# Performance work log

Measured on AMD Instinct MI355X. Metric: run time of the kernel, lower is better.

Reference implementation:

```python
import jax, jax.numpy as jnp
import numpy as np

N = 30000   # fluid particles
E = 480000  # edges
F = 4       # fluidFeatures (in channels)
P = 8       # RBF basis size per dim (dims=[8], 1D)
LAYERS = [32, 64, 64, 2]


def hat_basis(x, n):
    # 'linear' RBF: hat functions on n evenly spaced centers in [-1, 1]
    centers = jnp.linspace(-1.0, 1.0, n, dtype=x.dtype)
    spacing = 2.0 / (n - 1)
    return jnp.maximum(0.0, 1.0 - jnp.abs(x[:, None] - centers[None, :]) / spacing)  # [E, n]


def rbf_conv(x, fi, fj, d, W, b, mask, n_nodes):
    # x: [N, Cin]; d: [E, 1] clamped; W: [P, Cin, Cout]; b: [Cout]
    phi = hat_basis(d[:, 0], W.shape[0])      # [E, P]
    xj = x[fj]                                 # gather source features [E, Cin]
    msg = jnp.zeros((xj.shape[0], W.shape[2]), dtype=x.dtype)
    for p in range(W.shape[0]):                # small fixed P=8 loop keeps memory O(E*Cout)
        msg = msg + phi[:, p, None] * (xj @ W[p])
    msg = jnp.where(mask[:, None], msg, 0.0)   # centerIgnore: drop self edges fi==fj
    out = jax.ops.segment_sum(msg, fi, num_segments=n_nodes)  # scatter-reduce to targets
    return out + b


def _xavier(key, shape_in, shape_out):
    lim = float(np.sqrt(6.0 / (shape_in + shape_out)))
    return jax.random.uniform(key, (shape_in, shape_out), jnp.float32, -lim, lim)


def setup_inputs() -> dict:
    key = jax.random.key(0)
    ks = jax.random.split(key, 16)
    fluidFeatures = jax.random.normal(ks[0], (N, F), jnp.float32)
    fi = jax.random.randint(ks[1], (E,), 0, N)
    fj = jax.random.randint(ks[2], (E,), 0, N)
    distances = jax.random.normal(ks[3], (E, 1), jnp.float32)
    # conv channels: 4->32, 64->64, 64->64, 64->2
    cio = [(F, 32), (2 * 32, 64), (64, 64), (64, 2)]
    inp = {"fluidFeatures": fluidFeatures, "fi": fi, "fj": fj, "distances": distances}
    for li, (ci, co) in enumerate(cio):
        inp[f"cW{li}"] = jax.random.normal(ks[4 + li], (P, ci, co), jnp.float32) * (1.0 / np.sqrt(P * ci))
        inp[f"cb{li}"] = jnp.zeros((co,), jnp.float32)
        inp[f"fW{li}"] = _xavier(ks[8 + li], ci, co)   # stored [in, out]
        inp[f"fb{li}"] = jnp.zeros((co,), jnp.float32)
    return inp


def reference(fluidFeatures, fi, fj, distances,
              cW0, cb0, fW0, fb0, cW1, cb1, fW1, fb1,
              cW2, cb2, fW2, fb2, cW3, cb3, fW3, fb3):
    n_nodes = fluidFeatures.shape[0]
    mask = fi != fj                     # centerIgnore (mask instead of filter: jit-safe)
    d = jnp.clip(distances, -1.0, 1.0)

    conv0 = rbf_conv(fluidFeatures, fi, fj, d, cW0, cb0, mask, n_nodes)  # [N, 32]
    lin0 = fluidFeatures @ fW0 + fb0                                      # [N, 32]
    ans = jnp.concatenate([lin0, conv0], axis=1)                          # [N, 64]

    # i = 1: features[0]=32 != features[1]=64 -> no residual
    ansc = jax.nn.relu(ans)
    ans = rbf_conv(ansc, fi, fj, d, cW1, cb1, mask, n_nodes) + (ansc @ fW1 + fb1)
    # i = 2: features[1]==features[2]==64 and shapes match -> residual
    ansc = jax.nn.relu(ans)
    ans = rbf_conv(ansc, fi, fj, d, cW2, cb2, mask, n_nodes) + (ansc @ fW2 + fb2) + ans
    # i = 3: 64 -> 2, no residual
    ansc = jax.nn.relu(ans)
    ans = rbf_conv(ansc, fi, fj, d, cW3, cb3, mask, n_nodes) + (ansc @ fW3 + fb3)

    return ans  # dim == 1 (dims=[8]) -> no /128
```

## Files before the change

### kernel.cpp

```cpp
#include <hip/hip_runtime.h>


#define CAP 48

typedef __attribute__((ext_vector_type(8))) short short8;
typedef __attribute__((ext_vector_type(4))) short short4v;
typedef __attribute__((ext_vector_type(4))) float f32x4;

__device__ __forceinline__ short bf16s(float f) {
  unsigned u = __float_as_uint(f);
  return (short)((u + 0x7FFF + ((u >> 16) & 1)) >> 16);
}
__device__ __forceinline__ float b2f(unsigned short s) {
  return __uint_as_float(((unsigned)s) << 16);
}

__global__ void fill_kernel(const float* __restrict__ dist,
                            const int* __restrict__ fi, const int* __restrict__ fj,
                            int* __restrict__ cnt, int* __restrict__ jw, int nE) {
  int e = blockIdx.x * blockDim.x + threadIdx.x;
  if (e >= nE) return;
  int i = fi[e], j = fj[e];
  if (i == j) return;
  float d = fminf(1.0f, fmaxf(-1.0f, dist[e]));
  float u = (d + 1.0f) * 3.5f;
  int p = min((int)u, 6);
  float w0 = 1.0f - (u - (float)p);
  int wq = (int)(w0 * 16383.0f + 0.5f);
  int pos = atomicAdd(&cnt[i], 1);
  if (pos < CAP)
    jw[(size_t)i * CAP + pos] = j | (p << 15) | (wq << 18);
}

__global__ void prep_wtul(const float* __restrict__ cW1, const float* __restrict__ fW1,
                          const float* __restrict__ cW2, const float* __restrict__ fW2,
                          short* __restrict__ wt1, short* __restrict__ wt2) {
  int idx = blockIdx.x * blockDim.x + threadIdx.x;
  if (idx >= 2 * 576 * 64) return;
  int sel = idx / (576 * 64);
  int r = idx - sel * (576 * 64);
  int col = r >> 6, ch = r & 63;
  const float* cW = sel ? cW2 : cW1;
  const float* fW = sel ? fW2 : fW1;
  float v;
  if (col < 512) {
    int p = col >> 6, co = col & 63;
    v = cW[((size_t)p * 64 + ch) * 64 + co];
  } else {
    v = fW[(size_t)ch * 64 + (col - 512)];
  }
  (sel ? wt2 : wt1)[(size_t)col * 64 + ch] = bf16s(v);
}

__global__ __launch_bounds__(256) void layer0_kernel(
    const float* __restrict__ X,
    const int* __restrict__ cnt, const int* __restrict__ jw,
    const float* __restrict__ cW0,
    const float* __restrict__ cb0,
    const float* __restrict__ fW0,
    const float* __restrict__ fb0,
    unsigned short* __restrict__ ansc0, int n) {
  __shared__ float sW[1024];
  __shared__ float sF[128];
  __shared__ float sB[64];
  __shared__ float sacc[4][32];
  for (int idx = threadIdx.x; idx < 1024; idx += 256) sW[idx] = cW0[idx];
  for (int idx = threadIdx.x; idx < 128; idx += 256) sF[idx] = fW0[idx];
  if (threadIdx.x < 32) sB[threadIdx.x] = cb0[threadIdx.x];
  else if (threadIdx.x < 64) sB[threadIdx.x] = fb0[threadIdx.x - 32];
  const int w = threadIdx.x >> 6;
  const int lane = threadIdx.x & 63;
  const int i = blockIdx.x * 4 + w;
  const bool valid = (i < n);
  if (valid && lane < 32) sacc[w][lane] = 0.0f;
  __syncthreads();
  if (valid && lane < min(cnt[i], CAP)) {
    int v = jw[(size_t)i * CAP + lane];
    int j = v & 0x7FFF;
    int p = (v >> 15) & 7;
    float w0 = (float)((unsigned)v >> 18) * (1.0f / 16383.0f);
    float w1 = 1.0f - w0;
    float4 x = *(const float4*)(X + (size_t)j * 4);
    atomicAdd(&sacc[w][p * 4 + 0], w0 * x.x);
    atomicAdd(&sacc[w][p * 4 + 1], w0 * x.y);
    atomicAdd(&sacc[w][p * 4 + 2], w0 * x.z);
    atomicAdd(&sacc[w][p * 4 + 3], w0 * x.w);
    atomicAdd(&sacc[w][(p + 1) * 4 + 0], w1 * x.x);
    atomicAdd(&sacc[w][(p + 1) * 4 + 1], w1 * x.y);
    atomicAdd(&sacc[w][(p + 1) * 4 + 2], w1 * x.z);
    atomicAdd(&sacc[w][(p + 1) * 4 + 3], w1 * x.w);
  }
  __syncthreads();
  if (!valid) return;
  const float4 xi = *(const float4*)(X + (size_t)i * 4);
  float v;
  if (lane < 32) {
    v = sB[32 + lane];
    v = fmaf(xi.x, sF[0 * 32 + lane], v);
    v = fmaf(xi.y, sF[1 * 32 + lane], v);
    v = fmaf(xi.z, sF[2 * 32 + lane], v);
    v = fmaf(xi.w, sF[3 * 32 + lane], v);
  } else {
    const int cc = lane - 32;
    v = sB[cc];
    #pragma unroll
    for (int k = 0; k < 32; ++k)
      v = fmaf(sacc[w][k], sW[k * 32 + cc], v);
  }
  ansc0[(size_t)i * 64 + lane] = (unsigned short)bf16s(fmaxf(v, 0.0f));
}

__global__ __launch_bounds__(256) void gemm_ul(
    const unsigned short* __restrict__ Xb,
    const short* __restrict__ WTul,
    unsigned short* __restrict__ UL, int n) {
  __shared__ short sUL[16 * 584];
  const int lane = threadIdx.x & 63;
  const int w = threadIdx.x >> 6;
  const int mrow = lane & 15;
  const int quad = lane >> 4;
  const int nodeBase = blockIdx.x * 16;
  const int bnode = min(nodeBase + mrow, n - 1);
  const unsigned short* bBase = Xb + (size_t)bnode * 64 + quad * 8;
  short8 b0 = *(const short8*)(bBase);
  short8 b1 = *(const short8*)(bBase + 32);
  #pragma unroll
  for (int t = 0; t < 9; ++t) {
    const int ct = w * 9 + t;
    const short* aBase = WTul + (size_t)(ct * 16 + mrow) * 64 + quad * 8;
    short8 a0 = *(const short8*)(aBase);
    short8 a1 = *(const short8*)(aBase + 32);
    f32x4 acc = {0, 0, 0, 0};
    acc = __builtin_amdgcn_mfma_f32_16x16x32_bf16(a0, b0, acc, 0, 0, 0);
    acc = __builtin_amdgcn_mfma_f32_16x16x32_bf16(a1, b1, acc, 0, 0, 0);
    short4v pk;
    #pragma unroll
    for (int reg = 0; reg < 4; ++reg) pk[reg] = bf16s(acc[reg]);
    *(short4v*)(sUL + mrow * 584 + ct * 16 + quad * 4) = pk;
  }
  __syncthreads();
  const int r = threadIdx.x >> 4;
  const int c0 = threadIdx.x & 15;
  if (nodeBase + r < n) {
    unsigned short* dst = UL + (size_t)(nodeBase + r) * 576;
    #pragma unroll
    for (int chunk = c0; chunk < 72; chunk += 16)
      *(short8*)(dst + chunk * 8) = *(const short8*)(sUL + r * 584 + chunk * 8);
  }
}

template <bool HAS_RES, bool STORE_ANS>
__global__ __launch_bounds__(256) void conv_gather(
    const unsigned short* __restrict__ UL,
    const int* __restrict__ cnt, const int* __restrict__ jw,
    const float* __restrict__ cb, const float* __restrict__ fb,
    const float* __restrict__ resid,
    float* __restrict__ outAns,
    unsigned short* __restrict__ outAnsc, int n) {
  const int lane = threadIdx.x & 63;
  const int i = (blockIdx.x * blockDim.x + threadIdx.x) >> 6;
  if (i >= n) return;
  int rec = jw[(size_t)i * CAP + (lane < CAP ? lane : 0)];
  const int m = min(cnt[i], CAP);
  float acc = 0.0f;
  for (int q0 = 0; q0 < m; q0 += 16) {
    float u0[16], u1[16], w0s[16];
    #pragma unroll
    for (int k = 0; k < 16; ++k) {
      int v = __builtin_amdgcn_readlane(rec, q0 + k);
      int j = min(v & 0x7FFF, n - 1);
      int p = (v >> 15) & 7;
      w0s[k] = (float)((unsigned)v >> 18) * (1.0f / 16383.0f);
      const unsigned short* base = UL + (size_t)j * 576 + p * 64 + lane;
      u0[k] = b2f(base[0]);
      u1[k] = b2f(base[64]);
    }
    #pragma unroll
    for (int k = 0; k < 16; ++k) {
      bool ok = (q0 + k < m);
      float w0 = ok ? w0s[k] : 0.0f;
      float w1 = ok ? (1.0f - w0s[k]) : 0.0f;
      acc = fmaf(w0, u0[k], acc);
      acc = fmaf(w1, u1[k], acc);
    }
  }
  float L = b2f(UL[(size_t)i * 576 + 512 + lane]);
  float o = acc + L + cb[lane] + fb[lane];
  if (HAS_RES) o += resid[(size_t)i * 64 + lane];
  if (STORE_ANS) outAns[(size_t)i * 64 + lane] = o;
  outAnsc[(size_t)i * 64 + lane] = (unsigned short)bf16s(fmaxf(o, 0.0f));
}

__global__ __launch_bounds__(256) void prep_t(
    const unsigned short* __restrict__ Xb,
    const float* __restrict__ cW3,
    float* __restrict__ T, int n) {
  int idx = blockIdx.x * blockDim.x + threadIdx.x;
  if (idx >= n * 8) return;
  int i = idx >> 3, p = idx & 7;
  const unsigned short* xr = Xb + (size_t)i * 64;
  const float* wr = cW3 + p * 128;
  float s0 = 0.0f, s1 = 0.0f;
  #pragma unroll 16
  for (int ch = 0; ch < 64; ++ch) {
    float x = b2f(xr[ch]);
    s0 = fmaf(x, wr[ch * 2 + 0], s0);
    s1 = fmaf(x, wr[ch * 2 + 1], s1);
  }
  T[(size_t)i * 16 + p * 2 + 0] = s0;
  T[(size_t)i * 16 + p * 2 + 1] = s1;
}

__global__ __launch_bounds__(256, 4) void layer3_kernel(
    const unsigned short* __restrict__ Xb,
    const float* __restrict__ T,
    const int* __restrict__ cnt, const int* __restrict__ jw,
    const float* __restrict__ cb3, const float* __restrict__ fb3,
    const float* __restrict__ fW3,
    float* __restrict__ out, int n) {
  const int lane = threadIdx.x & 63;
  const int i = (blockIdx.x * blockDim.x + threadIdx.x) >> 6;
  if (i >= n) return;
  const int m = min(cnt[i], CAP);
  float c0 = 0.0f, c1 = 0.0f;
  if (lane < m) {
    int v = jw[(size_t)i * CAP + lane];
    int j = min(v & 0x7FFF, n - 1);
    int p = (v >> 15) & 7;
    float w0 = (float)((unsigned)v >> 18) * (1.0f / 16383.0f);
    float w1 = 1.0f - w0;
    const float* tb = T + (size_t)j * 16 + p * 2;
    float2 ta = *(const float2*)(tb);
    float2 tc = *(const float2*)(tb + 2);
    c0 = w0 * ta.x + w1 * tc.x;
    c1 = w0 * ta.y + w1 * tc.y;
  }
  float xi = b2f(Xb[(size_t)i * 64 + lane]);
  float2 fw = *(const float2*)(fW3 + lane * 2);
  c0 = fmaf(xi, fw.x, c0);
  c1 = fmaf(xi, fw.y, c1);
  #pragma unroll
  for (int off = 32; off > 0; off >>= 1) {
    c0 += __shfl_xor(c0, off, 64);
    c1 += __shfl_xor(c1, off, 64);
  }
  if (lane == 0) {
    out[(size_t)i * 2 + 0] = c0 + cb3[0] + fb3[0];
    out[(size_t)i * 2 + 1] = c1 + cb3[1] + fb3[1];
  }
}

extern "C" void kernel_launch(void* const* d_in, const int* in_sizes, int n_in,
                              void* d_out, int out_size, void* d_ws, size_t ws_size,
                              hipStream_t stream) {
  const float* X    = (const float*)d_in[0];
  const int*   fi   = (const int*)d_in[1];
  const int*   fj   = (const int*)d_in[2];
  const float* dist = (const float*)d_in[3];
  const float* cW0 = (const float*)d_in[4];  const float* cb0 = (const float*)d_in[5];
  const float* fW0 = (const float*)d_in[6];  const float* fb0 = (const float*)d_in[7];
  const float* cW1 = (const float*)d_in[8];  const float* cb1 = (const float*)d_in[9];
  const float* fW1 = (const float*)d_in[10]; const float* fb1 = (const float*)d_in[11];
  const float* cW2 = (const float*)d_in[12]; const float* cb2 = (const float*)d_in[13];
  const float* fW2 = (const float*)d_in[14]; const float* fb2 = (const float*)d_in[15];
  const float* cW3 = (const float*)d_in[16]; const float* cb3 = (const float*)d_in[17];
  const float* fW3 = (const float*)d_in[18]; const float* fb3 = (const float*)d_in[19];
  float* out = (float*)d_out;

  const int n  = in_sizes[0] / 4;
  const int nE = in_sizes[1];

  unsigned short* UL    = (unsigned short*)d_ws;
  unsigned short* ansc0 = UL + (size_t)n * 576;
  unsigned short* ansc1 = ansc0 + (size_t)n * 64;
  float*          ans1  = (float*)(ansc1 + (size_t)n * 64);
  unsigned short* ansc2 = ansc0;
  float* T     = ans1 + (size_t)n * 64;
  short* wtul1 = (short*)(T + (size_t)n * 16);
  short* wtul2 = wtul1 + 576 * 64;
  int*   jw    = (int*)(wtul2 + 576 * 64);
  int*   cnt   = jw + (size_t)n * CAP;

  hipMemsetAsync(cnt, 0, (size_t)n * sizeof(int), stream);
  fill_kernel<<<(nE + 255) / 256, 256, 0, stream>>>(dist, fi, fj, cnt, jw, nE);
  prep_wtul<<<(2 * 576 * 64 + 255) / 256, 256, 0, stream>>>(cW1, fW1, cW2, fW2, wtul1, wtul2);

  layer0_kernel<<<(n + 3) / 4, 256, 0, stream>>>(X, cnt, jw,
                                                 cW0, cb0, fW0, fb0, ansc0, n);
  gemm_ul<<<(n + 15) / 16, 256, 0, stream>>>(ansc0, wtul1, UL, n);
  conv_gather<false, true><<<(n * 64 + 255) / 256, 256, 0, stream>>>(
      UL, cnt, jw, cb1, fb1, nullptr, ans1, ansc1, n);
  gemm_ul<<<(n + 15) / 16, 256, 0, stream>>>(ansc1, wtul2, UL, n);
  conv_gather<true, false><<<(n * 64 + 255) / 256, 256, 0, stream>>>(
      UL, cnt, jw, cb2, fb2, ans1, nullptr, ansc2, n);
  prep_t<<<(n * 8 + 255) / 256, 256, 0, stream>>>(ansc2, cW3, T, n);
  layer3_kernel<<<(n * 64 + 255) / 256, 256, 0, stream>>>(ansc2, T, cnt, jw,
                                                          cb3, fb3, fW3, out, n);
}
```

Baseline: 276.4 us.

## Split per-node gather across two waves and fuse layer-3 T precompute

Each node's edge list is now split between two wavefronts, each covering up to 24 neighbors, and the two partial sums are combined through shared memory. This shortens each wave's serial gather chain and raises memory-level parallelism. The layer-2 gather also computes the layer-3 per-node projection T with a wave-wide shuffle reduction, which removes the separate prep_t kernel and its reread of ansc2. The costs are a block-wide barrier, half the waves sitting idle during the epilogue, and a 16-value shuffle reduction per node.

```diff
diff --git a/kernel.cpp b/kernel.cpp
--- a/kernel.cpp
+++ b/kernel.cpp
@@ -149,66 +149,78 @@
   }
 }
 
-template <bool HAS_RES, bool STORE_ANS>
+template <bool HAS_RES, bool STORE_ANS, bool COMPUTE_T>
 __global__ __launch_bounds__(256) void conv_gather(
     const unsigned short* __restrict__ UL,
     const int* __restrict__ cnt, const int* __restrict__ jw,
     const float* __restrict__ cb, const float* __restrict__ fb,
     const float* __restrict__ resid,
+    const float* __restrict__ cW3,
+    float* __restrict__ T,
     float* __restrict__ outAns,
     unsigned short* __restrict__ outAnsc, int n) {
+  __shared__ float sacc[2][64];
   const int lane = threadIdx.x & 63;
-  const int i = (blockIdx.x * blockDim.x + threadIdx.x) >> 6;
-  if (i >= n) return;
-  int rec = jw[(size_t)i * CAP + (lane < CAP ? lane : 0)];
-  const int m = min(cnt[i], CAP);
+  const int w = threadIdx.x >> 6;
+  const int nl = w >> 1, half = w & 1;
+  const int i = blockIdx.x * 2 + nl;
+  const bool valid = (i < n);
   float acc = 0.0f;
-  for (int q0 = 0; q0 < m; q0 += 16) {
-    float u0[16], u1[16], w0s[16];
-    #pragma unroll
-    for (int k = 0; k < 16; ++k) {
-      int v = __builtin_amdgcn_readlane(rec, q0 + k);
-      int j = min(v & 0x7FFF, n - 1);
-      int p = (v >> 15) & 7;
-      w0s[k] = (float)((unsigned)v >> 18) * (1.0f / 16383.0f);
-      const unsigned short* base = UL + (size_t)j * 576 + p * 64 + lane;
-      u0[k] = b2f(base[0]);
-      u1[k] = b2f(base[64]);
+  int span = 0;
+  if (valid) {
+    const int m = min(cnt[i], CAP);
+    span = min(max(m - half * 24, 0), 24);
+    int rec = jw[(size_t)i * CAP + half * 24 + (lane < 24 ? lane : 0)];
+    for (int q0 = 0; q0 < span; q0 += 16) {
+      float u0[16], u1[16], w0s[16];
+      #pragma unroll
+      for (int k = 0; k < 16; ++k) {
+        int v = __builtin_amdgcn_readlane(rec, (q0 + k) < 24 ? (q0 + k) : 0);
+        int j = min(v & 0x7FFF, n - 1);
+        int p = (v >> 15) & 7;
+        w0s[k] = (float)((unsigned)v >> 18) * (1.0f / 16383.0f);
+        const unsigned short* base = UL + (size_t)j * 576 + p * 64 + lane;
+        u0[k] = b2f(base[0]);
+        u1[k] = b2f(base[64]);
+      }
+      #pragma unroll
+      for (int k = 0; k < 16; ++k) {
+        bool ok = (q0 + k < span);
+        float w0 = ok ? w0s[k] : 0.0f;
+        float w1 = ok ? (1.0f - w0s[k]) : 0.0f;
+        acc = fmaf(w0, u0[k], acc);
+        acc = fmaf(w1, u1[k], acc);
+      }
     }
-    #pragma unroll
-    for (int k = 0; k < 16; ++k) {
-      bool ok = (q0 + k < m);
-      float w0 = ok ? w0s[k] : 0.0f;
-      float w1 = ok ? (1.0f - w0s[k]) : 0.0f;
-      acc = fmaf(w0, u0[k], acc);
-      acc = fmaf(w1, u1[k], acc);
+  }
+  if (half == 0) sacc[nl][lane] = acc;
+  __syncthreads();
+  if (half == 1 && valid) {
+    float total = acc + sacc[nl][lane];
+    float L = b2f(UL[(size_t)i * 576 + 512 + lane]);
+    float o = total + L + cb[lane] + fb[lane];
+    if (HAS_RES) o += resid[(size_t)i * 64 + lane];
+    if (STORE_ANS) outAns[(size_t)i * 64 + lane] = o;
+    unsigned short xb = (unsigned short)bf16s(fmaxf(o, 0.0f));
+    outAnsc[(size_t)i * 64 + lane] = xb;
+    if (COMPUTE_T) {
+      float x = b2f(xb);
+      float c[16];
+      #pragma unroll
+      for (int t = 0; t < 16; ++t)
+        c[t] = x * cW3[((size_t)(t >> 1) * 64 + lane) * 2 + (t & 1)];
+      #pragma unroll
+      for (int off = 32; off > 0; off >>= 1) {
+        #pragma unroll
+        for (int t = 0; t < 16; ++t) c[t] += __shfl_xor(c[t], off, 64);
+      }
+      if (lane == 0) {
+        float* tr = T + (size_t)i * 16;
+        #pragma unroll
+        for (int t = 0; t < 16; ++t) tr[t] = c[t];
+      }
     }
   }
-  float L = b2f(UL[(size_t)i * 576 + 512 + lane]);
-  float o = acc + L + cb[lane] + fb[lane];
-  if (HAS_RES) o += resid[(size_t)i * 64 + lane];
-  if (STORE_ANS) outAns[(size_t)i * 64 + lane] = o;
-  outAnsc[(size_t)i * 64 + lane] = (unsigned short)bf16s(fmaxf(o, 0.0f));
-}
-
-__global__ __launch_bounds__(256) void prep_t(
-    const unsigned short* __restrict__ Xb,
-    const float* __restrict__ cW3,
-    float* __restrict__ T, int n) {
-  int idx = blockIdx.x * blockDim.x + threadIdx.x;
-  if (idx >= n * 8) return;
-  int i = idx >> 3, p = idx & 7;
-  const unsigned short* xr = Xb + (size_t)i * 64;
-  const float* wr = cW3 + p * 128;
-  float s0 = 0.0f, s1 = 0.0f;
-  #pragma unroll 16
-  for (int ch = 0; ch < 64; ++ch) {
-    float x = b2f(xr[ch]);
-    s0 = fmaf(x, wr[ch * 2 + 0], s0);
-    s1 = fmaf(x, wr[ch * 2 + 1], s1);
-  }
-  T[(size_t)i * 16 + p * 2 + 0] = s0;
-  T[(size_t)i * 16 + p * 2 + 1] = s1;
 }
 
 __global__ __launch_bounds__(256, 4) void layer3_kernel(
@@ -288,12 +300,11 @@
   layer0_kernel<<<(n + 3) / 4, 256, 0, stream>>>(X, cnt, jw,
                                                  cW0, cb0, fW0, fb0, ansc0, n);
   gemm_ul<<<(n + 15) / 16, 256, 0, stream>>>(ansc0, wtul1, UL, n);
-  conv_gather<false, true><<<(n * 64 + 255) / 256, 256, 0, stream>>>(
-      UL, cnt, jw, cb1, fb1, nullptr, ans1, ansc1, n);
+  conv_gather<false, true, false><<<(n + 1) / 2, 256, 0, stream>>>(
+      UL, cnt, jw, cb1, fb1, nullptr, nullptr, nullptr, ans1, ansc1, n);
   gemm_ul<<<(n + 15) / 16, 256, 0, stream>>>(ansc1, wtul2, UL, n);
-  conv_gather<true, false><<<(n * 64 + 255) / 256, 256, 0, stream>>>(
-      UL, cnt, jw, cb2, fb2, ans1, nullptr, ansc2, n);
-  prep_t<<<(n * 8 + 255) / 256, 256, 0, stream>>>(ansc2, cW3, T, n);
+  conv_gather<true, false, true><<<(n + 1) / 2, 256, 0, stream>>>(
+      UL, cnt, jw, cb2, fb2, ans1, cW3, T, nullptr, ansc2, n);
   layer3_kernel<<<(n * 64 + 255) / 256, 256, 0, stream>>>(ansc2, T, cnt, jw,
                                                           cb3, fb3, fW3, out, n);
 }
```

Result: slower. 285.0 us (+3.1%).
